# Kernel optimization log

Measured on AMD Instinct MI355X. Metric: run time of the kernel, lower is better.

The kernel has to match this reference:

```python
import jax, jax.numpy as jnp
import numpy as np

N = 20000   # nodes
E = 320000  # edges (before self-loops)
D = 128     # hidden_dim (= per-head out channels, concat=False)
H = 4       # heads
NEG_SLOPE = 0.2   # GATv2 leaky_relu default
LN_EPS = 1e-5


def setup_inputs() -> dict:
    key = jax.random.key(0)
    ks = jax.random.split(key, 12)
    s = 0.05
    w = lambda k, shp: (jax.random.normal(k, shp, jnp.float32) * s)
    return {
        "x": jax.random.normal(ks[0], (N, D), jnp.float32),
        "src": jax.random.randint(ks[1], (E,), 0, N, jnp.int32),
        "dst": jax.random.randint(ks[2], (E,), 0, N, jnp.int32),
        "Wl1": w(ks[3], (D, H * D)), "Wr1": w(ks[4], (D, H * D)),
        "att1": w(ks[5], (H, D)), "b1": jnp.zeros((D,), jnp.float32),
        "g1": jnp.ones((D,), jnp.float32), "be1": jnp.zeros((D,), jnp.float32),
        "Wl2": w(ks[6], (D, H * D)), "Wr2": w(ks[7], (D, H * D)),
        "att2": w(ks[8], (H, D)), "b2": jnp.zeros((D,), jnp.float32),
        "g2": jnp.ones((D,), jnp.float32), "be2": jnp.zeros((D,), jnp.float32),
    }


def gatv2_conv(x, src, dst, Wl, Wr, att, bias):
    """GATv2Conv with concat=False (mean over heads), share_weights=False."""
    n = x.shape[0]
    xl = (x @ Wl).reshape(n, H, D)  # source-side projection
    xr = (x @ Wr).reshape(n, H, D)  # target-side projection
    m = jax.nn.leaky_relu(xl[src] + xr[dst], NEG_SLOPE)     # [E', H, D]
    e = jnp.einsum('ehd,hd->eh', m, att)                     # [E', H]
    # segment softmax over edges grouped by destination node
    e_max = jax.ops.segment_max(e, dst, num_segments=n)      # [N, H]
    ex = jnp.exp(e - e_max[dst])
    denom = jax.ops.segment_sum(ex, dst, num_segments=n)     # [N, H]
    alpha = ex / (denom[dst] + 1e-16)                        # [E', H]
    out = jax.ops.segment_sum(alpha[:, :, None] * xl[src], dst, num_segments=n)
    return out.mean(axis=1) + bias                           # [N, D]


def layer_norm(x, g, b):
    mu = x.mean(axis=-1, keepdims=True)
    var = ((x - mu) ** 2).mean(axis=-1, keepdims=True)
    return (x - mu) * jax.lax.rsqrt(var + LN_EPS) * g + b


def reference(x, src, dst, Wl1, Wr1, att1, b1, g1, be1,
              Wl2, Wr2, att2, b2, g2, be2):
    n = x.shape[0]
    # PyG GATv2Conv default add_self_loops=True
    loops = jnp.arange(n, dtype=src.dtype)
    s = jnp.concatenate([src, loops])
    d = jnp.concatenate([dst, loops])

    h = gatv2_conv(x, s, d, Wl1, Wr1, att1, b1)
    h = layer_norm(h, g1, be1)
    h = jax.nn.relu(h + x)

    h2 = gatv2_conv(h, s, d, Wl2, Wr2, att2, b2)
    h2 = layer_norm(h2, g2, be2)
    return h2 + h
```

## Files before the change

kernel.cpp:

```cpp
#include <hip/hip_runtime.h>
#include <hip/hip_bf16.h>
#include <hip/hip_fp16.h>

#define NNODES 20000
#define MPAD   20480
#define NEDGES 320000
#define DIM    128
#define NH     4
#define ETOT   (NEDGES + NNODES)
#define LN_EPS 1e-5f

typedef unsigned char  u8;
typedef unsigned short u16;
typedef unsigned int   u32;

typedef _Float16    f16x2 __attribute__((ext_vector_type(2)));
typedef _Float16    f16x8 __attribute__((ext_vector_type(8)));
typedef float       f32x2 __attribute__((ext_vector_type(2)));
typedef float       f32x4 __attribute__((ext_vector_type(4)));

__device__ inline u16 f2h(float f) {
    _Float16 h = (_Float16)f;
    union { _Float16 h; u16 u; } v; v.h = h; return v.u;
}
__device__ inline _Float16 bits2h(u16 b) {
    union { u16 u; _Float16 h; } v; v.u = b; return v.h;
}
__device__ inline f16x2 u2h2(u32 u) { union { u32 u; f16x2 h; } v; v.u = u; return v.h; }
__device__ inline u32 h22u(f16x2 h) { union { f16x2 h; u32 u; } v; v.h = h; return v.u; }
__device__ inline f16x2 habs2(f16x2 h) { return u2h2(h22u(h) & 0x7FFF7FFFu); }

#define GLDS16(g, l) __builtin_amdgcn_global_load_lds(                         \
    (const __attribute__((address_space(1))) void*)(g),                        \
    (__attribute__((address_space(3))) void*)(l), 16, 0, 0)


__global__ __launch_bounds__(256) void k_prep(const float* __restrict__ x, u16* __restrict__ xb,
                       const float* __restrict__ Wl1, const float* __restrict__ Wr1,
                       u16* __restrict__ Bt1,
                       const float* __restrict__ Wl2, const float* __restrict__ Wr2,
                       u16* __restrict__ Bt2,
                       int* __restrict__ deg) {
    const int b = blockIdx.x, t = threadIdx.x;
    const int gid = b * 256 + t;
    if (gid < NNODES) deg[gid] = 1;

    for (int j = gid; j < NNODES * 32; j += 256 * 256) {
        float4 v = ((const float4*)x)[j];
        ushort4 o;
        o.x = f2h(v.x); o.y = f2h(v.y); o.z = f2h(v.z); o.w = f2h(v.w);
        ((ushort4*)xb)[j] = o;
    }

    {
        const int m    = b >> 6;
        const int tile = b & 63;
        const int kt   = tile >> 4;
        const int nt   = tile & 15;
        const float* W = (m == 0) ? Wl1 : (m == 1) ? Wr1 : (m == 2) ? Wl2 : Wr2;
        u16* Bt        = (m < 2) ? Bt1 : Bt2;
        const int nbase = (m & 1) * 512 + nt * 32;

        __shared__ float lds[32][33];
        const int tx = t & 31, ty = t >> 5;
#pragma unroll
        for (int i = 0; i < 4; ++i) {
            int k = kt * 32 + ty + i * 8;
            lds[ty + i * 8][tx] = W[k * 512 + nt * 32 + tx];
        }
        __syncthreads();
#pragma unroll
        for (int i = 0; i < 4; ++i) {
            int nrow = nbase + ty + i * 8;
            Bt[nrow * 128 + kt * 32 + tx] = f2h(lds[tx][ty + i * 8]);
        }
    }
}


__global__ void k_hist(const int* __restrict__ dst, int* __restrict__ deg) {
    int i = blockIdx.x * blockDim.x + threadIdx.x;
    if (i < NEDGES) atomicAdd(&deg[dst[i]], 1);
}

__global__ __launch_bounds__(1024) void k_scan(const int* __restrict__ deg,
                                               int* __restrict__ row,
                                               int* __restrict__ cur) {
    __shared__ int part[1024];
    const int CH = 20;
    int t = threadIdx.x;
    int base = t * CH;
    int s = 0;
    int d[20];
    if (base < NNODES) {
#pragma unroll
        for (int q = 0; q < 5; ++q) {
            int4 v = ((const int4*)(deg + base))[q];
            d[q*4+0] = v.x; d[q*4+1] = v.y; d[q*4+2] = v.z; d[q*4+3] = v.w;
            s += v.x + v.y + v.z + v.w;
        }
    }
    part[t] = s;
    __syncthreads();
    for (int off = 1; off < 1024; off <<= 1) {
        int v = (t >= off) ? part[t - off] : 0;
        __syncthreads();
        part[t] += v;
        __syncthreads();
    }
    if (base < NNODES) {
        int run = (t == 0) ? 0 : part[t - 1];
#pragma unroll
        for (int i = 0; i < CH; i++) {
            row[base + i] = run; cur[base + i] = run; run += d[i];
        }
    }
    if (t == 1023) row[NNODES] = part[1023];
}

__global__ void k_scatter(const int* __restrict__ src, const int* __restrict__ dst,
                          int* __restrict__ col, int* __restrict__ cur) {
    int i = blockIdx.x * blockDim.x + threadIdx.x;
    if (i < NEDGES) {
        int d = dst[i];
        int pos = atomicAdd(&cur[d], 1);
        col[pos] = src[i];
    } else if (i < ETOT) {
        int n = i - NEDGES;
        int pos = atomicAdd(&cur[n], 1);
        col[pos] = n;
    }
}


__global__ __launch_bounds__(256, 2) void k_gemm_f16(const u16* __restrict__ A,
                                                     const u16* __restrict__ Bt,
                                                     u8*  __restrict__ XLq,
                                                     u16* __restrict__ scales,
                                                     u16* __restrict__ XR) {
    __shared__ u16 smA[128 * 128];
    __shared__ u16 smB[128 * 128];
    const int L   = blockIdx.x;
    const int xcd = L & 7;
    const int w9  = L >> 3;
    const int bm  = (xcd * 20 + (w9 >> 3)) * 128;
    const int bn  = (w9 & 7) * 128;
    const int t  = threadIdx.x;
    const int w  = t >> 6;
    const int l  = t & 63;

    {
        char* smAb = (char*)smA;
        char* smBb = (char*)smB;
#pragma unroll
        for (int p = 0; p < 8; ++p) {
            int rbase = w * 32 + p * 4;
            int row   = rbase + (l >> 4);
            int j     = (l & 15) ^ (row & 7);
            const u16* ga = A  + (size_t)(bm + row) * 128 + j * 8;
            const u16* gb = Bt + (size_t)(bn + row) * 128 + j * 8;
            GLDS16(ga, smAb + rbase * 256);
            GLDS16(gb, smBb + rbase * 256);
        }
    }
    __syncthreads();

    const int wr  = (w >> 1) * 64;
    const int wc  = (w & 1) * 64;
    const int lr  = l & 15;
    const int lkb = (l >> 4) * 16;

    f32x4 acc[4][4] = {};

#pragma unroll
    for (int ks = 0; ks < 4; ++ks) {
        f16x8 af[4], bfr[4];
#pragma unroll
        for (int i = 0; i < 4; ++i) {
            int ra = wr + i * 16 + lr;
            af[i]  = *(const f16x8*)((const char*)smA +
                        ((ra * 256 + ks * 64 + lkb) ^ ((ra & 7) << 4)));
            int rb = wc + i * 16 + lr;
            bfr[i] = *(const f16x8*)((const char*)smB +
                        ((rb * 256 + ks * 64 + lkb) ^ ((rb & 7) << 4)));
        }
#pragma unroll
        for (int mi = 0; mi < 4; ++mi)
#pragma unroll
            for (int ni = 0; ni < 4; ++ni)
                acc[mi][ni] = __builtin_amdgcn_mfma_f32_16x16x32_f16(
                    bfr[ni], af[mi], acc[mi][ni], 0, 0, 0);
    }

    __syncthreads();
    u16* smC = smA;
    {
        const int n4 = (l >> 4) * 4;
#pragma unroll
        for (int mi = 0; mi < 4; ++mi) {
            int m = wr + mi * 16 + lr;
#pragma unroll
            for (int ni = 0; ni < 4; ++ni) {
                int n = wc + ni * 16 + n4;
                f32x4 v = acc[mi][ni];
                ushort4 o;
                o.x = f2h(v[0]); o.y = f2h(v[1]); o.z = f2h(v[2]); o.w = f2h(v[3]);
                *(ushort4*)((char*)smC + (m * 256 + ((n * 2) ^ ((m & 7) << 4)))) = o;
            }
        }
    }
    __syncthreads();

    if (bn < 512) {
        const int head = bn >> 7;
        const int lr16 = l & 15;
        const int rg   = l >> 4;
#pragma unroll
        for (int p = 0; p < 8; ++p) {
            int r = w * 32 + p * 4 + rg;
            uint4 vv = *(const uint4*)((const char*)smC +
                        (r * 256 + ((lr16 * 16) ^ ((r & 7) << 4))));
            f32x2 c0 = __builtin_convertvector(u2h2(vv.x), f32x2);
            f32x2 c1 = __builtin_convertvector(u2h2(vv.y), f32x2);
            f32x2 c2 = __builtin_convertvector(u2h2(vv.z), f32x2);
            f32x2 c3 = __builtin_convertvector(u2h2(vv.w), f32x2);
            float f[8] = {c0[0],c0[1],c1[0],c1[1],c2[0],c2[1],c3[0],c3[1]};
            float m = 0.f;
#pragma unroll
            for (int k = 0; k < 8; ++k) m = fmaxf(m, fabsf(f[k]));
#pragma unroll
            for (int o = 1; o < 16; o <<= 1) m = fmaxf(m, __shfl_xor(m, o, 64));
            float inv = (m > 0.f) ? (127.f / m) : 0.f;
            int q[8];
#pragma unroll
            for (int k = 0; k < 8; ++k) {
                int qi = (int)__builtin_rintf(f[k] * inv);
                q[k] = qi > 127 ? 127 : (qi < -127 ? -127 : qi);
            }
            u32 lo = (q[0]&255) | ((q[1]&255)<<8) | ((q[2]&255)<<16) | ((q[3]&255)<<24);
            u32 hi = (q[4]&255) | ((q[5]&255)<<8) | ((q[6]&255)<<16) | ((q[7]&255)<<24);
            uint2 pk; pk.x = lo; pk.y = hi;
            *(uint2*)(XLq + (size_t)(bm + r) * 512 + head * 128 + lr16 * 8) = pk;
            if (lr16 == 0) scales[(bm + r) * 4 + head] = f2h(m * (1.f / 127.f));
        }
    } else {
        int r  = t >> 4;
        int cb = (t & 15) * 16;
        u16* base = XR + (bn - 512);
#pragma unroll
        for (int p = 0; p < 8; ++p) {
            int row = p * 16 + r;
            uint4 v = *(const uint4*)((const char*)smC +
                        (row * 256 + (cb ^ ((row & 7) << 4))));
            *(uint4*)(base + (size_t)(bm + row) * 512 + (cb >> 1)) = v;
        }
    }
}


__global__ __launch_bounds__(256) void k_attn(const u8*  __restrict__ XLq,
                                              const u16* __restrict__ scales,
                                              const u16* __restrict__ XR,
                                              const float* __restrict__ att,
                                              const float* __restrict__ bias,
                                              const float* __restrict__ gamma,
                                              const float* __restrict__ beta,
                                              const int* __restrict__ row,
                                              const int* __restrict__ col,
                                              const float* __restrict__ res,
                                              float* __restrict__ out,
                                              u16* __restrict__ out_h,
                                              int relu_flag) {
    const int wid = __builtin_amdgcn_readfirstlane(threadIdx.x >> 6);
    const int n   = blockIdx.x * 4 + wid;
    const int l   = threadIdx.x & 63;
    const int h   = l >> 4;
    const int e   = l & 15;

    const f16x2 C06 = {(_Float16)0.6f, (_Float16)0.6f};
    const f16x2 C04 = {(_Float16)0.4f, (_Float16)0.4f};
    const f16x2 M1152 = {(_Float16)(-1152.f), (_Float16)(-1152.f)};
    const u32 K64 = 0x64646464u;

    const int lane_off = h * 128 + e * 8;

    uint4 xru = *(const uint4*)(XR + (size_t)n * 512 + lane_off);
    f16x2 xr0 = u2h2(xru.x), xr1 = u2h2(xru.y), xr2 = u2h2(xru.z), xr3 = u2h2(xru.w);

    const float* ap = att + lane_off;
    float4 af0 = *(const float4*)(ap);
    float4 af1 = *(const float4*)(ap + 4);
    f16x2 at0 = {(_Float16)af0.x, (_Float16)af0.y};
    f16x2 at1 = {(_Float16)af0.z, (_Float16)af0.w};
    f16x2 at2 = {(_Float16)af1.x, (_Float16)af1.y};
    f16x2 at3 = {(_Float16)af1.z, (_Float16)af1.w};

    f16x2 acch[4] = {};
    float ssum = 0.f;

    const int beg = row[n], end = row[n + 1];

    for (int i = beg; i < end; i += 2) {
        int s0 = col[i];
        bool has2 = (i + 1 < end);
        int s1 = has2 ? col[i + 1] : s0;

        uint2 a0 = *(const uint2*)(XLq + (size_t)s0 * 512 + lane_off);
        uint2 a1 = *(const uint2*)(XLq + (size_t)s1 * 512 + lane_off);
        _Float16 sh0 = bits2h(scales[s0 * 4 + h]);
        _Float16 sh1 = bits2h(scales[s1 * 4 + h]);
        f16x2 s0h2 = {sh0, sh0};
        f16x2 s1h2 = {sh1, sh1};

        u32 w00 = a0.x ^ 0x80808080u, w01 = a0.y ^ 0x80808080u;
        u32 w10 = a1.x ^ 0x80808080u, w11 = a1.y ^ 0x80808080u;
        f16x2 q00 = u2h2(__builtin_amdgcn_perm(K64, w00, 0x04010400u)) + M1152;
        f16x2 q01 = u2h2(__builtin_amdgcn_perm(K64, w00, 0x04030402u)) + M1152;
        f16x2 q02 = u2h2(__builtin_amdgcn_perm(K64, w01, 0x04010400u)) + M1152;
        f16x2 q03 = u2h2(__builtin_amdgcn_perm(K64, w01, 0x04030402u)) + M1152;
        f16x2 q10 = u2h2(__builtin_amdgcn_perm(K64, w10, 0x04010400u)) + M1152;
        f16x2 q11 = u2h2(__builtin_amdgcn_perm(K64, w10, 0x04030402u)) + M1152;
        f16x2 q12 = u2h2(__builtin_amdgcn_perm(K64, w11, 0x04010400u)) + M1152;
        f16x2 q13 = u2h2(__builtin_amdgcn_perm(K64, w11, 0x04030402u)) + M1152;

        float e0, e1;
        {
            f16x2 v0 = q00 * s0h2 + xr0, v1 = q01 * s0h2 + xr1;
            f16x2 v2 = q02 * s0h2 + xr2, v3 = q03 * s0h2 + xr3;
            f16x2 k0 = v0 * C06 + habs2(v0) * C04;
            f16x2 k1 = v1 * C06 + habs2(v1) * C04;
            f16x2 k2 = v2 * C06 + habs2(v2) * C04;
            f16x2 k3 = v3 * C06 + habs2(v3) * C04;
            e0 = __builtin_amdgcn_fdot2(k0, at0, 0.f, false);
            e0 = __builtin_amdgcn_fdot2(k1, at1, e0, false);
            e0 = __builtin_amdgcn_fdot2(k2, at2, e0, false);
            e0 = __builtin_amdgcn_fdot2(k3, at3, e0, false);
        }
        {
            f16x2 v0 = q10 * s1h2 + xr0, v1 = q11 * s1h2 + xr1;
            f16x2 v2 = q12 * s1h2 + xr2, v3 = q13 * s1h2 + xr3;
            f16x2 k0 = v0 * C06 + habs2(v0) * C04;
            f16x2 k1 = v1 * C06 + habs2(v1) * C04;
            f16x2 k2 = v2 * C06 + habs2(v2) * C04;
            f16x2 k3 = v3 * C06 + habs2(v3) * C04;
            e1 = __builtin_amdgcn_fdot2(k0, at0, 0.f, false);
            e1 = __builtin_amdgcn_fdot2(k1, at1, e1, false);
            e1 = __builtin_amdgcn_fdot2(k2, at2, e1, false);
            e1 = __builtin_amdgcn_fdot2(k3, at3, e1, false);
        }

#pragma unroll
        for (int m = 1; m < 16; m <<= 1) {
            e0 += __shfl_xor(e0, m, 64);
            e1 += __shfl_xor(e1, m, 64);
        }

        float p0 = __expf(e0);
        float p1 = has2 ? __expf(e1) : 0.f;
        ssum += p0 + p1;

        _Float16 ph0s = (_Float16)(p0 * (float)sh0);
        _Float16 ph1s = (_Float16)(p1 * (float)sh1);
        f16x2 ph0 = {ph0s, ph0s};
        f16x2 ph1 = {ph1s, ph1s};
        acch[0] = acch[0] + ph0 * q00 + ph1 * q10;
        acch[1] = acch[1] + ph0 * q01 + ph1 * q11;
        acch[2] = acch[2] + ph0 * q02 + ph1 * q12;
        acch[3] = acch[3] + ph0 * q03 + ph1 * q13;
    }

    float acc[8];
    {
        f32x2 c;
        c = __builtin_convertvector(acch[0], f32x2); acc[0] = c[0]; acc[1] = c[1];
        c = __builtin_convertvector(acch[1], f32x2); acc[2] = c[0]; acc[3] = c[1];
        c = __builtin_convertvector(acch[2], f32x2); acc[4] = c[0]; acc[5] = c[1];
        c = __builtin_convertvector(acch[3], f32x2); acc[6] = c[0]; acc[7] = c[1];
    }
    float inv = 1.f / (ssum + 1e-16f);
#pragma unroll
    for (int jj = 0; jj < 8; ++jj) acc[jj] *= inv;
#pragma unroll
    for (int jj = 0; jj < 8; ++jj) acc[jj] += __shfl_xor(acc[jj], 16, 64);
#pragma unroll
    for (int jj = 0; jj < 8; ++jj) acc[jj] += __shfl_xor(acc[jj], 32, 64);

    if (h == 0) {
        const int dd = e * 8;
        float4 b40 = *(const float4*)(bias + dd);
        float4 b41 = *(const float4*)(bias + dd + 4);
        float y[8];
        y[0] = acc[0]*0.25f + b40.x; y[1] = acc[1]*0.25f + b40.y;
        y[2] = acc[2]*0.25f + b40.z; y[3] = acc[3]*0.25f + b40.w;
        y[4] = acc[4]*0.25f + b41.x; y[5] = acc[5]*0.25f + b41.y;
        y[6] = acc[6]*0.25f + b41.z; y[7] = acc[7]*0.25f + b41.w;

        float s1 = 0.f, s2 = 0.f;
#pragma unroll
        for (int jj = 0; jj < 8; ++jj) { s1 += y[jj]; s2 += y[jj]*y[jj]; }
#pragma unroll
        for (int m = 1; m < 16; m <<= 1) {
            s1 += __shfl_xor(s1, m, 64);
            s2 += __shfl_xor(s2, m, 64);
        }
        float mu = s1 * (1.f / 128.f);
        float var = s2 * (1.f / 128.f) - mu * mu;
        float rstd = rsqrtf(var + LN_EPS);

        float4 g40 = *(const float4*)(gamma + dd);
        float4 g41 = *(const float4*)(gamma + dd + 4);
        float4 e40 = *(const float4*)(beta + dd);
        float4 e41 = *(const float4*)(beta + dd + 4);
        float4 r40 = *(const float4*)(res + (size_t)n * 128 + dd);
        float4 r41 = *(const float4*)(res + (size_t)n * 128 + dd + 4);
        float g[8] = {g40.x,g40.y,g40.z,g40.w,g41.x,g41.y,g41.z,g41.w};
        float be[8] = {e40.x,e40.y,e40.z,e40.w,e41.x,e41.y,e41.z,e41.w};
        float r[8] = {r40.x,r40.y,r40.z,r40.w,r41.x,r41.y,r41.z,r41.w};
#pragma unroll
        for (int jj = 0; jj < 8; ++jj) {
            y[jj] = (y[jj] - mu) * rstd * g[jj] + be[jj] + r[jj];
            if (relu_flag) y[jj] = fmaxf(y[jj], 0.f);
        }
        float4 o0 = {y[0],y[1],y[2],y[3]};
        float4 o1 = {y[4],y[5],y[6],y[7]};
        *(float4*)(out + (size_t)n * 128 + dd)     = o0;
        *(float4*)(out + (size_t)n * 128 + dd + 4) = o1;
        if (out_h) {
            ushort4 oh0, oh1;
            oh0.x = f2h(y[0]); oh0.y = f2h(y[1]); oh0.z = f2h(y[2]); oh0.w = f2h(y[3]);
            oh1.x = f2h(y[4]); oh1.y = f2h(y[5]); oh1.z = f2h(y[6]); oh1.w = f2h(y[7]);
            *(ushort4*)(out_h + (size_t)n * 128 + dd)     = oh0;
            *(ushort4*)(out_h + (size_t)n * 128 + dd + 4) = oh1;
        }
    }
}


extern "C" void kernel_launch(void* const* d_in, const int* in_sizes, int n_in,
                              void* d_out, int out_size, void* d_ws, size_t ws_size,
                              hipStream_t stream) {
    const float* x    = (const float*)d_in[0];
    const int*   src  = (const int*)d_in[1];
    const int*   dst  = (const int*)d_in[2];
    const float* Wl1  = (const float*)d_in[3];
    const float* Wr1  = (const float*)d_in[4];
    const float* att1 = (const float*)d_in[5];
    const float* b1   = (const float*)d_in[6];
    const float* g1   = (const float*)d_in[7];
    const float* be1  = (const float*)d_in[8];
    const float* Wl2  = (const float*)d_in[9];
    const float* Wr2  = (const float*)d_in[10];
    const float* att2 = (const float*)d_in[11];
    const float* b2   = (const float*)d_in[12];
    const float* g2   = (const float*)d_in[13];
    const float* be2  = (const float*)d_in[14];
    float* out = (float*)d_out;

    char* ws = (char*)d_ws;
    size_t off = 0;
    u8*    xlq  = (u8*)(ws + off);    off += (size_t)MPAD * 512;
    u16*   scl  = (u16*)(ws + off);   off += (size_t)MPAD * 4 * 2;
    u16*   xrb  = (u16*)(ws + off);   off += (size_t)MPAD * 512 * 2;
    u16*   xb   = (u16*)(ws + off);   off += (size_t)MPAD * 128 * 2;
    float* hbuf = (float*)(ws + off); off += (size_t)NNODES * 128 * 4;
    u16*   Bt1  = (u16*)(ws + off);   off += (size_t)1024 * 128 * 2;
    u16*   Bt2  = (u16*)(ws + off);   off += (size_t)1024 * 128 * 2;
    int*   deg  = (int*)(ws + off);   off += (size_t)NNODES * 4;
    int*   rowp = (int*)(ws + off);   off += (size_t)(NNODES + 1) * 4;
    int*   cur  = (int*)(ws + off);   off += (size_t)NNODES * 4;
    int*   col  = (int*)(ws + off);   off += (size_t)ETOT * 4;

    k_prep<<<256, 256, 0, stream>>>(x, xb, Wl1, Wr1, Bt1, Wl2, Wr2, Bt2, deg);
    k_hist<<<(NEDGES + 255) / 256, 256, 0, stream>>>(dst, deg);
    k_scan<<<1, 1024, 0, stream>>>(deg, rowp, cur);
    k_scatter<<<(ETOT + 255) / 256, 256, 0, stream>>>(src, dst, col, cur);

    k_gemm_f16<<<MPAD / 128 * 8, 256, 0, stream>>>(xb, Bt1, xlq, scl, xrb);
    k_attn<<<NNODES / 4, 256, 0, stream>>>(xlq, scl, xrb, att1, b1, g1, be1, rowp, col,
                                           x, hbuf, xb, 1);
    k_gemm_f16<<<MPAD / 128 * 8, 256, 0, stream>>>(xb, Bt2, xlq, scl, xrb);
    k_attn<<<NNODES / 4, 256, 0, stream>>>(xlq, scl, xrb, att2, b2, g2, be2, rowp, col,
                                           hbuf, out, (u16*)nullptr, 0);
}
```

Measured before the change: 180.4 us.

## Split leaky_relu linear part into per-node precomputed att dot products

```diff
diff --git a/kernel.cpp b/kernel.cpp
--- a/kernel.cpp
+++ b/kernel.cpp
@@ -29,6 +29,19 @@
 __device__ inline f16x2 u2h2(u32 u) { union { u32 u; f16x2 h; } v; v.u = u; return v.h; }
 __device__ inline u32 h22u(f16x2 h) { union { f16x2 h; u32 u; } v; v.h = h; return v.u; }
 __device__ inline f16x2 habs2(f16x2 h) { return u2h2(h22u(h) & 0x7FFF7FFFu); }
+
+#define DPP_ROR(x, ctrl) ({ union {float f; int i;} _a, _b; _a.f=(x); \
+    _b.i = __builtin_amdgcn_update_dpp(0, _a.i, (ctrl), 0xF, 0xF, true); _b.f; })
+__device__ inline float rowsum16(float x) {
+    x += DPP_ROR(x, 0x121); x += DPP_ROR(x, 0x122);
+    x += DPP_ROR(x, 0x124); x += DPP_ROR(x, 0x128);
+    return x;
+}
+__device__ inline float rowmax16(float x) {
+    x = fmaxf(x, DPP_ROR(x, 0x121)); x = fmaxf(x, DPP_ROR(x, 0x122));
+    x = fmaxf(x, DPP_ROR(x, 0x124)); x = fmaxf(x, DPP_ROR(x, 0x128));
+    return x;
+}
 
 #define GLDS16(g, l) __builtin_amdgcn_global_load_lds(                         \
     (const __attribute__((address_space(1))) void*)(g),                        \
@@ -135,8 +148,10 @@
 
 __global__ __launch_bounds__(256, 2) void k_gemm_f16(const u16* __restrict__ A,
                                                      const u16* __restrict__ Bt,
+                                                     const float* __restrict__ att,
                                                      u8*  __restrict__ XLq,
-                                                     u16* __restrict__ scales,
+                                                     u32* __restrict__ sclD,
+                                                     u16* __restrict__ Dr6,
                                                      u16* __restrict__ XR) {
     __shared__ u16 smA[128 * 128];
     __shared__ u16 smB[128 * 128];
@@ -211,10 +226,15 @@
     }
     __syncthreads();
 
+    const int lr16 = l & 15;
+    const int rg   = l >> 4;
+    const int head = (bn < 512) ? (bn >> 7) : ((bn >> 7) - 4);
+    const float* ap = att + head * 128 + lr16 * 8;
+    float4 aa0 = *(const float4*)(ap);
+    float4 aa1 = *(const float4*)(ap + 4);
+    const float av[8] = {aa0.x, aa0.y, aa0.z, aa0.w, aa1.x, aa1.y, aa1.z, aa1.w};
+
     if (bn < 512) {
-        const int head = bn >> 7;
-        const int lr16 = l & 15;
-        const int rg   = l >> 4;
 #pragma unroll
         for (int p = 0; p < 8; ++p) {
             int r = w * 32 + p * 4 + rg;
@@ -225,11 +245,11 @@
             f32x2 c2 = __builtin_convertvector(u2h2(vv.z), f32x2);
             f32x2 c3 = __builtin_convertvector(u2h2(vv.w), f32x2);
             float f[8] = {c0[0],c0[1],c1[0],c1[1],c2[0],c2[1],c3[0],c3[1]};
-            float m = 0.f;
-#pragma unroll
-            for (int k = 0; k < 8; ++k) m = fmaxf(m, fabsf(f[k]));
-#pragma unroll
-            for (int o = 1; o < 16; o <<= 1) m = fmaxf(m, __shfl_xor(m, o, 64));
+            float m = 0.f, d = 0.f;
+#pragma unroll
+            for (int k = 0; k < 8; ++k) { m = fmaxf(m, fabsf(f[k])); d += f[k] * av[k]; }
+            m = rowmax16(m);
+            d = rowsum16(d);
             float inv = (m > 0.f) ? (127.f / m) : 0.f;
             int q[8];
 #pragma unroll
@@ -241,9 +261,27 @@
             u32 hi = (q[4]&255) | ((q[5]&255)<<8) | ((q[6]&255)<<16) | ((q[7]&255)<<24);
             uint2 pk; pk.x = lo; pk.y = hi;
             *(uint2*)(XLq + (size_t)(bm + r) * 512 + head * 128 + lr16 * 8) = pk;
-            if (lr16 == 0) scales[(bm + r) * 4 + head] = f2h(m * (1.f / 127.f));
+            if (lr16 == 0)
+                sclD[(bm + r) * 4 + head] =
+                    (u32)f2h(m * (1.f / 127.f)) | ((u32)f2h(0.6f * d) << 16);
         }
     } else {
+#pragma unroll
+        for (int p = 0; p < 8; ++p) {
+            int r = w * 32 + p * 4 + rg;
+            uint4 vv = *(const uint4*)((const char*)smC +
+                        (r * 256 + ((lr16 * 16) ^ ((r & 7) << 4))));
+            f32x2 c0 = __builtin_convertvector(u2h2(vv.x), f32x2);
+            f32x2 c1 = __builtin_convertvector(u2h2(vv.y), f32x2);
+            f32x2 c2 = __builtin_convertvector(u2h2(vv.z), f32x2);
+            f32x2 c3 = __builtin_convertvector(u2h2(vv.w), f32x2);
+            float f[8] = {c0[0],c0[1],c1[0],c1[1],c2[0],c2[1],c3[0],c3[1]};
+            float d = 0.f;
+#pragma unroll
+            for (int k = 0; k < 8; ++k) d += f[k] * av[k];
+            d = rowsum16(d);
+            if (lr16 == 0) Dr6[(bm + r) * 4 + head] = f2h(0.6f * d);
+        }
         int r  = t >> 4;
         int cb = (t & 15) * 16;
         u16* base = XR + (bn - 512);
@@ -259,7 +297,8 @@
 
 
 __global__ __launch_bounds__(256) void k_attn(const u8*  __restrict__ XLq,
-                                              const u16* __restrict__ scales,
+                                              const u32* __restrict__ sclD,
+                                              const u16* __restrict__ Dr6,
                                               const u16* __restrict__ XR,
                                               const float* __restrict__ att,
                                               const float* __restrict__ bias,
@@ -277,8 +316,6 @@
     const int h   = l >> 4;
     const int e   = l & 15;
 
-    const f16x2 C06 = {(_Float16)0.6f, (_Float16)0.6f};
-    const f16x2 C04 = {(_Float16)0.4f, (_Float16)0.4f};
     const f16x2 M1152 = {(_Float16)(-1152.f), (_Float16)(-1152.f)};
     const u32 K64 = 0x64646464u;
 
@@ -290,10 +327,12 @@
     const float* ap = att + lane_off;
     float4 af0 = *(const float4*)(ap);
     float4 af1 = *(const float4*)(ap + 4);
-    f16x2 at0 = {(_Float16)af0.x, (_Float16)af0.y};
-    f16x2 at1 = {(_Float16)af0.z, (_Float16)af0.w};
-    f16x2 at2 = {(_Float16)af1.x, (_Float16)af1.y};
-    f16x2 at3 = {(_Float16)af1.z, (_Float16)af1.w};
+    f16x2 at0 = {(_Float16)(0.4f*af0.x), (_Float16)(0.4f*af0.y)};
+    f16x2 at1 = {(_Float16)(0.4f*af0.z), (_Float16)(0.4f*af0.w)};
+    f16x2 at2 = {(_Float16)(0.4f*af1.x), (_Float16)(0.4f*af1.y)};
+    f16x2 at3 = {(_Float16)(0.4f*af1.z), (_Float16)(0.4f*af1.w)};
+
+    const float dr6n = (float)bits2h(Dr6[n * 4 + h]);
 
     f16x2 acch[4] = {};
     float ssum = 0.f;
@@ -307,8 +346,12 @@
 
         uint2 a0 = *(const uint2*)(XLq + (size_t)s0 * 512 + lane_off);
         uint2 a1 = *(const uint2*)(XLq + (size_t)s1 * 512 + lane_off);
-        _Float16 sh0 = bits2h(scales[s0 * 4 + h]);
-        _Float16 sh1 = bits2h(scales[s1 * 4 + h]);
+        u32 sd0 = sclD[s0 * 4 + h];
+        u32 sd1 = sclD[s1 * 4 + h];
+        _Float16 sh0 = bits2h((u16)sd0);
+        _Float16 sh1 = bits2h((u16)sd1);
+        float d60 = dr6n + (float)bits2h((u16)(sd0 >> 16));
+        float d61 = dr6n + (float)bits2h((u16)(sd1 >> 16));
         f16x2 s0h2 = {sh0, sh0};
         f16x2 s1h2 = {sh1, sh1};
 
@@ -327,36 +370,27 @@
         {
             f16x2 v0 = q00 * s0h2 + xr0, v1 = q01 * s0h2 + xr1;
             f16x2 v2 = q02 * s0h2 + xr2, v3 = q03 * s0h2 + xr3;
-            f16x2 k0 = v0 * C06 + habs2(v0) * C04;
-            f16x2 k1 = v1 * C06 + habs2(v1) * C04;
-            f16x2 k2 = v2 * C06 + habs2(v2) * C04;
-            f16x2 k3 = v3 * C06 + habs2(v3) * C04;
-            e0 = __builtin_amdgcn_fdot2(k0, at0, 0.f, false);
-            e0 = __builtin_amdgcn_fdot2(k1, at1, e0, false);
-            e0 = __builtin_amdgcn_fdot2(k2, at2, e0, false);
-            e0 = __builtin_amdgcn_fdot2(k3, at3, e0, false);
+            e0 = __builtin_amdgcn_fdot2(habs2(v0), at0, 0.f, false);
+            e0 = __builtin_amdgcn_fdot2(habs2(v1), at1, e0, false);
+            e0 = __builtin_amdgcn_fdot2(habs2(v2), at2, e0, false);
+            e0 = __builtin_amdgcn_fdot2(habs2(v3), at3, e0, false);
         }
         {
             f16x2 v0 = q10 * s1h2 + xr0, v1 = q11 * s1h2 + xr1;
             f16x2 v2 = q12 * s1h2 + xr2, v3 = q13 * s1h2 + xr3;
-            f16x2 k0 = v0 * C06 + habs2(v0) * C04;
-            f16x2 k1 = v1 * C06 + habs2(v1) * C04;
-            f16x2 k2 = v2 * C06 + habs2(v2) * C04;
-            f16x2 k3 = v3 * C06 + habs2(v3) * C04;
-            e1 = __builtin_amdgcn_fdot2(k0, at0, 0.f, false);
-            e1 = __builtin_amdgcn_fdot2(k1, at1, e1, false);
-            e1 = __builtin_amdgcn_fdot2(k2, at2, e1, false);
-            e1 = __builtin_amdgcn_fdot2(k3, at3, e1, false);
-        }
-
-#pragma unroll
-        for (int m = 1; m < 16; m <<= 1) {
-            e0 += __shfl_xor(e0, m, 64);
-            e1 += __shfl_xor(e1, m, 64);
-        }
-
-        float p0 = __expf(e0);
-        float p1 = has2 ? __expf(e1) : 0.f;
+            e1 = __builtin_amdgcn_fdot2(habs2(v0), at0, 0.f, false);
+            e1 = __builtin_amdgcn_fdot2(habs2(v1), at1, e1, false);
+            e1 = __builtin_amdgcn_fdot2(habs2(v2), at2, e1, false);
+            e1 = __builtin_amdgcn_fdot2(habs2(v3), at3, e1, false);
+        }
+
+        e0 += DPP_ROR(e0, 0x121); e1 += DPP_ROR(e1, 0x121);
+        e0 += DPP_ROR(e0, 0x122); e1 += DPP_ROR(e1, 0x122);
+        e0 += DPP_ROR(e0, 0x124); e1 += DPP_ROR(e1, 0x124);
+        e0 += DPP_ROR(e0, 0x128); e1 += DPP_ROR(e1, 0x128);
+
+        float p0 = __expf(e0 + d60);
+        float p1 = has2 ? __expf(e1 + d61) : 0.f;
         ssum += p0 + p1;
 
         _Float16 ph0s = (_Float16)(p0 * (float)sh0);
@@ -459,7 +493,8 @@
     char* ws = (char*)d_ws;
     size_t off = 0;
     u8*    xlq  = (u8*)(ws + off);    off += (size_t)MPAD * 512;
-    u16*   scl  = (u16*)(ws + off);   off += (size_t)MPAD * 4 * 2;
+    u32*   scld = (u32*)(ws + off);   off += (size_t)MPAD * 4 * 4;
+    u16*   dr6  = (u16*)(ws + off);   off += (size_t)MPAD * 4 * 2;
     u16*   xrb  = (u16*)(ws + off);   off += (size_t)MPAD * 512 * 2;
     u16*   xb   = (u16*)(ws + off);   off += (size_t)MPAD * 128 * 2;
     float* hbuf = (float*)(ws + off); off += (size_t)NNODES * 128 * 4;
@@ -475,10 +510,10 @@
     k_scan<<<1, 1024, 0, stream>>>(deg, rowp, cur);
     k_scatter<<<(ETOT + 255) / 256, 256, 0, stream>>>(src, dst, col, cur);
 
-    k_gemm_f16<<<MPAD / 128 * 8, 256, 0, stream>>>(xb, Bt1, xlq, scl, xrb);
-    k_attn<<<NNODES / 4, 256, 0, stream>>>(xlq, scl, xrb, att1, b1, g1, be1, rowp, col,
-                                           x, hbuf, xb, 1);
-    k_gemm_f16<<<MPAD / 128 * 8, 256, 0, stream>>>(xb, Bt2, xlq, scl, xrb);
-    k_attn<<<NNODES / 4, 256, 0, stream>>>(xlq, scl, xrb, att2, b2, g2, be2, rowp, col,
-                                           hbuf, out, (u16*)nullptr, 0);
-}
+    k_gemm_f16<<<MPAD / 128 * 8, 256, 0, stream>>>(xb, Bt1, att1, xlq, scld, dr6, xrb);
+    k_attn<<<NNODES / 4, 256, 0, stream>>>(xlq, scld, dr6, xrb, att1, b1, g1, be1,
+                                           rowp, col, x, hbuf, xb, 1);
+    k_gemm_f16<<<MPAD / 128 * 8, 256, 0, stream>>>(xb, Bt2, att2, xlq, scld, dr6, xrb);
+    k_attn<<<NNODES / 4, 256, 0, stream>>>(xlq, scld, dr6, xrb, att2, b2, g2, be2,
+                                           rowp, col, hbuf, out, (u16*)nullptr, 0);
+}
```

After: 174.1 us. -3.5%, faster.
